# Kernel tuning notes

Measured on AMD Instinct MI355X. Metric: run time of the kernel, lower is better.

## Reference

```python
import jax, jax.numpy as jnp
import numpy as np
from jax import lax

B, C_IN, H, W = 8, 64, 256, 256
C_OUT = 128
M = 800000      # number of pixel mappings
V = 200000      # number of views (atomic groups)
N = 50000       # number of 3D points (view groups)


def _csr_ptr(key, n_seg, total):
    inner = jnp.sort(jax.random.randint(key, (n_seg - 1,), 0, total + 1, dtype=jnp.int32))
    return jnp.concatenate([jnp.zeros((1,), jnp.int32), inner,
                            jnp.full((1,), total, jnp.int32)])


def setup_inputs() -> dict:
    key = jax.random.key(0)
    k = jax.random.split(key, 7)
    x = jax.random.normal(k[0], (B, C_IN, H, W), jnp.float32)
    w = jax.random.normal(k[1], (C_OUT, C_IN, 3, 3), jnp.float32) * (1.0 / np.sqrt(C_IN * 9))
    b = jax.random.normal(k[2], (C_OUT,), jnp.float32) * 0.01
    x_3d = jax.random.normal(k[3], (N, C_OUT), jnp.float32)
    n_flat = B * (H // 2) * (W // 2)  # flattened down-conv output pixels
    fm_idx = jax.random.randint(k[4], (M,), 0, n_flat, dtype=jnp.int32)
    a_ptr = _csr_ptr(k[5], V, M)
    v_ptr = _csr_ptr(k[6], N, V)
    return {"x": x, "w": w, "b": b, "x_3d": x_3d,
            "fm_idx": fm_idx, "a_ptr": a_ptr, "v_ptr": v_ptr}


def _csr_segment_max(feats, ptr, num_segments):
    # CSR pointers -> per-row segment ids (jit-safe), then segment max.
    seg = jnp.searchsorted(ptr, jnp.arange(feats.shape[0], dtype=ptr.dtype), side='right') - 1
    out = jax.ops.segment_max(feats, seg, num_segments=num_segments)
    return jnp.where(jnp.isfinite(out), out, 0.0)  # empty segments -> 0


def reference(x, w, b, x_3d, fm_idx, a_ptr, v_ptr):
    # conv down (stride 2, pad 1) + ReLU
    y = lax.conv_general_dilated(x, w, (2, 2), ((1, 1), (1, 1)),
                                 dimension_numbers=('NCHW', 'OIHW', 'NCHW'))
    y = jax.nn.relu(y + b[None, :, None, None])
    # feature map indexing: flat gather of mapped pixels -> [M, C]
    flat = y.transpose(0, 2, 3, 1).reshape(-1, y.shape[1])
    g = flat[fm_idx]
    # atomic pool: pixels -> views (CSR segment max)
    xv = _csr_segment_max(g, a_ptr, V)
    # view pool: views -> 3D points (CSR segment max)
    xp = _csr_segment_max(xv, v_ptr, N)
    # additive fusion
    return x_3d + xp
```

## Files before the change

### kernel.cpp

```cpp
#include <hip/hip_runtime.h>
#include <hip/hip_bf16.h>


#define B_IMG  8
#define C_IN   64
#define H_IN   256
#define W_IN   256
#define C_OUT  128
#define OH     128
#define OW     128
#define NPIX   (B_IMG * OH * OW)
#define KTOT   576
#define N_PTS  50000

#define HP     258
#define PLANE  (129 * 64)
#define HROW   (2 * PLANE)

typedef __bf16 bf16x8 __attribute__((ext_vector_type(8)));
typedef float  f32x4  __attribute__((ext_vector_type(4)));

typedef unsigned int __attribute__((address_space(3))) u32_lds;
typedef unsigned int __attribute__((address_space(1))) u32_glb;

#define GLOAD_LDS16(gsrc, ldst)                                                \
  __builtin_amdgcn_global_load_lds((const u32_glb*)(gsrc),                     \
                                   (u32_lds*)(ldst), 16, 0, 0)

#define XTP_BYTES   (B_IMG * HP * HROW * 2)
#define G_BYTES     (NPIX * C_OUT * 2)
#define XTP_OFF     0
#define G_OFF       XTP_BYTES
#define WT2_OFF     (XTP_BYTES + G_BYTES)

__global__ __launch_bounds__(256) void zero_ws_kernel(uint4* __restrict__ p, long n16) {
  long i = (long)blockIdx.x * blockDim.x + threadIdx.x;
  long stride = (long)gridDim.x * blockDim.x;
  uint4 z = make_uint4(0u, 0u, 0u, 0u);
  for (; i < n16; i += stride) p[i] = z;
}

__global__ __launch_bounds__(256) void transpose_x_kernel(
    const float* __restrict__ x, __hip_bfloat16* __restrict__ xtp) {
  __shared__ __hip_bfloat16 tile[64][66];
  const int tid = threadIdx.x;
  const int w0  = blockIdx.x * 64;
  const int h   = blockIdx.y;
  const int b   = blockIdx.z;

  const int wl  = tid & 63;
  const int ci4 = tid >> 6;
  for (int cc = 0; cc < 16; ++cc) {
    int ci = cc * 4 + ci4;
    float v = x[(((long)(b * C_IN + ci) * H_IN) + h) * W_IN + w0 + wl];
    tile[ci][wl] = (__hip_bfloat16)v;
  }
  __syncthreads();
  const int cl  = tid & 63;
  const int wo4 = tid >> 6;
  const long rowbase = ((long)(b * HP) + h + 1) * HROW;
  for (int wc = 0; wc < 16; ++wc) {
    int wloc = wc * 4 + wo4;
    int pc   = w0 + wloc + 1;
    xtp[rowbase + (pc & 1) * PLANE + (pc >> 1) * 64 + cl] = tile[cl][wloc];
  }
}

__global__ __launch_bounds__(256) void wprep_kernel(
    const float* __restrict__ w, __hip_bfloat16* __restrict__ wt2b) {
  int tid  = blockIdx.x * 256 + threadIdx.x;
  int khkw = tid >> 13;
  int cout = (tid >> 6) & 127;
  int ci   = tid & 63;
  wt2b[tid] = (__hip_bfloat16)w[(cout * C_IN + ci) * 9 + khkw];
}

__global__ __launch_bounds__(256) void conv_gemm_kernel(
    const __hip_bfloat16* __restrict__ xtp,
    const __hip_bfloat16* __restrict__ wt2b,
    const float* __restrict__ bias,
    __hip_bfloat16* __restrict__ g) {
  __shared__ __hip_bfloat16 Abuf[2][8192];
  __shared__ __hip_bfloat16 Bbuf[2][8192];

  const int tid  = threadIdx.x;
  const int lane = tid & 63;
  const int wid  = tid >> 6;
  const int bid  = blockIdx.x;
  const int bimg = bid >> 7;
  const int oh   = bid & 127;
  const int wr   = wid >> 1;
  const int wc   = wid & 1;

  f32x4 acc[4][4] = {};

  auto stage = [&](int buf, int t) {
    const int kh = t / 3;
    const int kw = t - kh * 3;
    const long abase = (((long)bimg * HP + (2 * oh + kh)) * 2 + (kw & 1)) * PLANE
                       + ((kw == 2) ? 64 : 0);
    const long bbase = (long)t * 8192;
    for (int p = 0; p < 4; ++p) {
      int flat = p * 256 + tid;
      int row  = flat >> 3;
      int cs   = (flat & 7) ^ (row & 7);
      long soff = (long)row * 64 + cs * 8;
      char* dA = (char*)&Abuf[buf][0] + flat * 16;
      char* dB = (char*)&Bbuf[buf][0] + flat * 16;
      GLOAD_LDS16(xtp + abase + soff, dA);
      GLOAD_LDS16(wt2b + bbase + soff, dB);
    }
  };

  auto compute = [&](int buf) {
    const int r15 = lane & 15;
    const int kg  = lane >> 4;
    for (int h = 0; h < 2; ++h) {
      bf16x8 af[4], bfv[4];
      const int co = h * 4 + kg;
      for (int i = 0; i < 4; ++i) {
        int rowa = wr * 64 + i * 16 + r15;
        int ca   = co ^ (rowa & 7);
        af[i] = *(const bf16x8*)((const char*)&Abuf[buf][0] + rowa * 128 + ca * 16);
        int rowb = wc * 64 + i * 16 + r15;
        int cb   = co ^ (rowb & 7);
        bfv[i] = *(const bf16x8*)((const char*)&Bbuf[buf][0] + rowb * 128 + cb * 16);
      }
      for (int i = 0; i < 4; ++i)
        for (int n = 0; n < 4; ++n)
          acc[i][n] = __builtin_amdgcn_mfma_f32_16x16x32_bf16(af[i], bfv[n],
                                                              acc[i][n], 0, 0, 0);
    }
  };

  stage(0, 0);
  __syncthreads();
  int cur = 0;
  for (int t = 0; t < 9; ++t) {
    if (t + 1 < 9) stage(cur ^ 1, t + 1);
    compute(cur);
    __syncthreads();
    cur ^= 1;
  }

  __hip_bfloat16* ct = &Abuf[0][0];
  const int col0 = wc * 64 + (lane & 15);
  float bn[4];
  for (int n = 0; n < 4; ++n) bn[n] = bias[col0 + n * 16];
  for (int i = 0; i < 4; ++i) {
    int row0 = wr * 64 + i * 16 + (lane >> 4) * 4;
    for (int n = 0; n < 4; ++n) {
      int cout = col0 + n * 16;
      for (int r = 0; r < 4; ++r) {
        float v = fmaxf(acc[i][n][r] + bn[n], 0.0f);
        ct[(row0 + r) * 128 + cout] = (__hip_bfloat16)v;
      }
    }
  }
  __syncthreads();
  const long gbase = (long)bid * (128 * 128);
  for (int it = 0; it < 8; ++it) {
    int flat = it * 256 + tid;
    bf16x8 v = *(const bf16x8*)((const char*)ct + flat * 16);
    *(bf16x8*)(g + gbase + (long)flat * 8) = v;
  }
}

__global__ __launch_bounds__(256) void gather_max_add_kernel(
    const __hip_bfloat16* __restrict__ g,
    const float* __restrict__ x3d,
    const int* __restrict__ fm_idx,
    const int* __restrict__ a_ptr,
    const int* __restrict__ v_ptr,
    float* __restrict__ out) {
  const int lane = threadIdx.x & 63;
  const int n    = blockIdx.x * 4 + (threadIdx.x >> 6);

  const int v0 = v_ptr[n];
  const int v1 = v_ptr[n + 1];
  const int r0 = a_ptr[v0];
  const int r1 = a_ptr[v1];
  const int len = r1 - r0;

  const int sub  = lane >> 4;
  const int ch16 = lane & 15;

  float m[8];
#pragma unroll
  for (int k = 0; k < 8; ++k) m[k] = 0.0f;

  const uint4* gp = (const uint4*)g;

  for (int base = 0; base < len; base += 64) {
    int nb = len - base;
    if (nb > 64) nb = 64;
    int li = base + lane;
    if (li >= len) li = len - 1;
    const int idx_l = fm_idx[r0 + li];

    for (int j = 0; j < nb; j += 8) {
      int ra = j + sub;
      int rb = j + 4 + sub;
      if (ra >= nb) ra = nb - 1;
      if (rb >= nb) rb = nb - 1;
      int ia = __shfl(idx_l, ra);
      int ib = __shfl(idx_l, rb);
      uint4 va = gp[(long)ia * 16 + ch16];
      uint4 vb = gp[(long)ib * 16 + ch16];
      const unsigned* ua = (const unsigned*)&va;
      const unsigned* ub = (const unsigned*)&vb;
#pragma unroll
      for (int w = 0; w < 4; ++w) {
        m[2 * w]     = fmaxf(m[2 * w],     __uint_as_float(ua[w] << 16));
        m[2 * w + 1] = fmaxf(m[2 * w + 1], __uint_as_float(ua[w] & 0xffff0000u));
        m[2 * w]     = fmaxf(m[2 * w],     __uint_as_float(ub[w] << 16));
        m[2 * w + 1] = fmaxf(m[2 * w + 1], __uint_as_float(ub[w] & 0xffff0000u));
      }
    }
  }

#pragma unroll
  for (int k = 0; k < 8; ++k) {
    m[k] = fmaxf(m[k], __shfl_xor(m[k], 16));
    m[k] = fmaxf(m[k], __shfl_xor(m[k], 32));
  }

  if (sub == 0) {
    const float4* x4 = (const float4*)x3d;
    float4* o4 = (float4*)out;
    long b0 = (long)n * 32 + ch16 * 2;
    float4 xa = x4[b0];
    float4 xb = x4[b0 + 1];
    float4 oa, ob;
    oa.x = xa.x + m[0]; oa.y = xa.y + m[1]; oa.z = xa.z + m[2]; oa.w = xa.w + m[3];
    ob.x = xb.x + m[4]; ob.y = xb.y + m[5]; ob.z = xb.z + m[6]; ob.w = xb.w + m[7];
    o4[b0]     = oa;
    o4[b0 + 1] = ob;
  }
}

extern "C" void kernel_launch(void* const* d_in, const int* in_sizes, int n_in,
                              void* d_out, int out_size, void* d_ws, size_t ws_size,
                              hipStream_t stream) {
  const float* x     = (const float*)d_in[0];
  const float* w     = (const float*)d_in[1];
  const float* bias  = (const float*)d_in[2];
  const float* x3d   = (const float*)d_in[3];
  const int*   fmidx = (const int*)d_in[4];
  const int*   aptr  = (const int*)d_in[5];
  const int*   vptr  = (const int*)d_in[6];
  float* out = (float*)d_out;

  char* ws = (char*)d_ws;
  __hip_bfloat16* xtp  = (__hip_bfloat16*)(ws + XTP_OFF);
  __hip_bfloat16* g    = (__hip_bfloat16*)(ws + G_OFF);
  __hip_bfloat16* wt2b = (__hip_bfloat16*)(ws + WT2_OFF);

  long n16 = XTP_BYTES / 16;
  hipLaunchKernelGGL(zero_ws_kernel, dim3(4096), dim3(256), 0, stream,
                     (uint4*)xtp, n16);
  hipLaunchKernelGGL(transpose_x_kernel, dim3(W_IN / 64, H_IN, B_IMG), dim3(256),
                     0, stream, x, xtp);
  hipLaunchKernelGGL(wprep_kernel, dim3((C_OUT * KTOT) / 256), dim3(256), 0,
                     stream, w, wt2b);
  hipLaunchKernelGGL(conv_gemm_kernel, dim3(NPIX / 128), dim3(256), 0, stream,
                     xtp, wt2b, bias, g);
  hipLaunchKernelGGL(gather_max_add_kernel, dim3(N_PTS / 4), dim3(256), 0,
                     stream, g, x3d, fmidx, aptr, vptr, out);
}
```

Measured before the change: 304.4 us.

## Zero only halo, pack transpose stores, widen conv blocks, split gather across warps

Replaces the full workspace zeroing with a kernel that clears only the padding rows and columns. The input transpose now packs two bf16 channels into 32-bit LDS and global stores. The conv GEMM uses 512-thread blocks with 8 waves, each owning a 64x32 output tile instead of 64x64. The gather/segment-max kernel assigns one block per 3D point, splits the rows across four waves, and reduces the partial maxima through shared memory. Together these aim to cut redundant memory traffic and raise parallelism, at the cost of more blocks and an extra sync in the gather.

After: 346.0 us. +13.7%, slower.

```diff
diff --git a/kernel.cpp b/kernel.cpp
--- a/kernel.cpp
+++ b/kernel.cpp
@@ -33,36 +33,49 @@
 #define G_OFF       XTP_BYTES
 #define WT2_OFF     (XTP_BYTES + G_BYTES)
 
-__global__ __launch_bounds__(256) void zero_ws_kernel(uint4* __restrict__ p, long n16) {
-  long i = (long)blockIdx.x * blockDim.x + threadIdx.x;
-  long stride = (long)gridDim.x * blockDim.x;
+__global__ __launch_bounds__(256) void halo_zero_kernel(__hip_bfloat16* __restrict__ xtp) {
+  const int ph = blockIdx.x;
+  const int b  = blockIdx.y;
+  const int tid = threadIdx.x;
+  const long base = ((long)b * HP + ph) * HROW;
   uint4 z = make_uint4(0u, 0u, 0u, 0u);
-  for (; i < n16; i += stride) p[i] = z;
+  uint4* p = (uint4*)(xtp + base);
+  if (ph == 0 || ph == HP - 1) {
+    for (int i = tid; i < (HROW * 2) / 16; i += 256) p[i] = z;
+  } else {
+    if (tid < 8) p[tid] = z;
+    else if (tid < 16) ((uint4*)(xtp + base + PLANE + 128 * 64))[tid - 8] = z;
+  }
 }
 
 __global__ __launch_bounds__(256) void transpose_x_kernel(
-    const float* __restrict__ x, __hip_bfloat16* __restrict__ xtp) {
-  __shared__ __hip_bfloat16 tile[64][66];
+    const float* __restrict__ x, unsigned* __restrict__ xtp32) {
+  __shared__ unsigned tile32[32][65];
   const int tid = threadIdx.x;
   const int w0  = blockIdx.x * 64;
   const int h   = blockIdx.y;
   const int b   = blockIdx.z;
 
-  const int wl  = tid & 63;
-  const int ci4 = tid >> 6;
-  for (int cc = 0; cc < 16; ++cc) {
-    int ci = cc * 4 + ci4;
-    float v = x[(((long)(b * C_IN + ci) * H_IN) + h) * W_IN + w0 + wl];
-    tile[ci][wl] = (__hip_bfloat16)v;
-  }
-  __syncthreads();
-  const int cl  = tid & 63;
-  const int wo4 = tid >> 6;
-  const long rowbase = ((long)(b * HP) + h + 1) * HROW;
-  for (int wc = 0; wc < 16; ++wc) {
-    int wloc = wc * 4 + wo4;
+  const int wl = tid & 63;
+  const int c4 = tid >> 6;
+  for (int cc = 0; cc < 8; ++cc) {
+    int cpair = cc * 4 + c4;
+    const float* xr = x + (((long)(b * C_IN + 2 * cpair) * H_IN) + h) * W_IN + w0;
+    float v0 = xr[wl];
+    float v1 = xr[(long)H_IN * W_IN + wl];
+    unsigned u0 = __builtin_bit_cast(unsigned short, (__bf16)v0);
+    unsigned u1 = __builtin_bit_cast(unsigned short, (__bf16)v1);
+    tile32[cpair][wl] = u0 | (u1 << 16);
+  }
+  __syncthreads();
+  const int cpair = tid & 31;
+  const int ws0   = tid >> 5;
+  const long rowb2 = (((long)(b * HP) + h + 1) * HROW) >> 1;
+  for (int it = 0; it < 8; ++it) {
+    int wloc = it * 8 + ws0;
     int pc   = w0 + wloc + 1;
-    xtp[rowbase + (pc & 1) * PLANE + (pc >> 1) * 64 + cl] = tile[cl][wloc];
+    xtp32[rowb2 + (pc & 1) * (PLANE >> 1) + (pc >> 1) * 32 + cpair] =
+        tile32[cpair][wloc];
   }
 }
 
@@ -75,7 +88,7 @@
   wt2b[tid] = (__hip_bfloat16)w[(cout * C_IN + ci) * 9 + khkw];
 }
 
-__global__ __launch_bounds__(256) void conv_gemm_kernel(
+__global__ __launch_bounds__(512) void conv_gemm_kernel(
     const __hip_bfloat16* __restrict__ xtp,
     const __hip_bfloat16* __restrict__ wt2b,
     const float* __restrict__ bias,
@@ -89,10 +102,10 @@
   const int bid  = blockIdx.x;
   const int bimg = bid >> 7;
   const int oh   = bid & 127;
-  const int wr   = wid >> 1;
-  const int wc   = wid & 1;
-
-  f32x4 acc[4][4] = {};
+  const int wr   = wid >> 2;
+  const int wc   = wid & 3;
+
+  f32x4 acc[4][2] = {};
 
   auto stage = [&](int buf, int t) {
     const int kh = t / 3;
@@ -100,8 +113,8 @@
     const long abase = (((long)bimg * HP + (2 * oh + kh)) * 2 + (kw & 1)) * PLANE
                        + ((kw == 2) ? 64 : 0);
     const long bbase = (long)t * 8192;
-    for (int p = 0; p < 4; ++p) {
-      int flat = p * 256 + tid;
+    for (int p = 0; p < 2; ++p) {
+      int flat = p * 512 + tid;
       int row  = flat >> 3;
       int cs   = (flat & 7) ^ (row & 7);
       long soff = (long)row * 64 + cs * 8;
@@ -116,18 +129,20 @@
     const int r15 = lane & 15;
     const int kg  = lane >> 4;
     for (int h = 0; h < 2; ++h) {
-      bf16x8 af[4], bfv[4];
+      bf16x8 af[4], bfv[2];
       const int co = h * 4 + kg;
       for (int i = 0; i < 4; ++i) {
         int rowa = wr * 64 + i * 16 + r15;
         int ca   = co ^ (rowa & 7);
         af[i] = *(const bf16x8*)((const char*)&Abuf[buf][0] + rowa * 128 + ca * 16);
-        int rowb = wc * 64 + i * 16 + r15;
+      }
+      for (int n = 0; n < 2; ++n) {
+        int rowb = wc * 32 + n * 16 + r15;
         int cb   = co ^ (rowb & 7);
-        bfv[i] = *(const bf16x8*)((const char*)&Bbuf[buf][0] + rowb * 128 + cb * 16);
+        bfv[n] = *(const bf16x8*)((const char*)&Bbuf[buf][0] + rowb * 128 + cb * 16);
       }
       for (int i = 0; i < 4; ++i)
-        for (int n = 0; n < 4; ++n)
+        for (int n = 0; n < 2; ++n)
           acc[i][n] = __builtin_amdgcn_mfma_f32_16x16x32_bf16(af[i], bfv[n],
                                                               acc[i][n], 0, 0, 0);
     }
@@ -144,12 +159,12 @@
   }
 
   __hip_bfloat16* ct = &Abuf[0][0];
-  const int col0 = wc * 64 + (lane & 15);
-  float bn[4];
-  for (int n = 0; n < 4; ++n) bn[n] = bias[col0 + n * 16];
+  const int col0 = wc * 32 + (lane & 15);
+  float bn[2];
+  for (int n = 0; n < 2; ++n) bn[n] = bias[col0 + n * 16];
   for (int i = 0; i < 4; ++i) {
     int row0 = wr * 64 + i * 16 + (lane >> 4) * 4;
-    for (int n = 0; n < 4; ++n) {
+    for (int n = 0; n < 2; ++n) {
       int cout = col0 + n * 16;
       for (int r = 0; r < 4; ++r) {
         float v = fmaxf(acc[i][n][r] + bn[n], 0.0f);
@@ -159,8 +174,8 @@
   }
   __syncthreads();
   const long gbase = (long)bid * (128 * 128);
-  for (int it = 0; it < 8; ++it) {
-    int flat = it * 256 + tid;
+  for (int it = 0; it < 4; ++it) {
+    int flat = it * 512 + tid;
     bf16x8 v = *(const bf16x8*)((const char*)ct + flat * 16);
     *(bf16x8*)(g + gbase + (long)flat * 8) = v;
   }
@@ -173,8 +188,11 @@
     const int* __restrict__ a_ptr,
     const int* __restrict__ v_ptr,
     float* __restrict__ out) {
-  const int lane = threadIdx.x & 63;
-  const int n    = blockIdx.x * 4 + (threadIdx.x >> 6);
+  __shared__ float red[4][128];
+  const int tid  = threadIdx.x;
+  const int lane = tid & 63;
+  const int wid  = tid >> 6;
+  const int n    = blockIdx.x;
 
   const int v0 = v_ptr[n];
   const int v1 = v_ptr[n + 1];
@@ -191,7 +209,7 @@
 
   const uint4* gp = (const uint4*)g;
 
-  for (int base = 0; base < len; base += 64) {
+  for (int base = wid * 64; base < len; base += 256) {
     int nb = len - base;
     if (nb > 64) nb = 64;
     int li = base + lane;
@@ -224,18 +242,16 @@
     m[k] = fmaxf(m[k], __shfl_xor(m[k], 16));
     m[k] = fmaxf(m[k], __shfl_xor(m[k], 32));
   }
-
   if (sub == 0) {
-    const float4* x4 = (const float4*)x3d;
-    float4* o4 = (float4*)out;
-    long b0 = (long)n * 32 + ch16 * 2;
-    float4 xa = x4[b0];
-    float4 xb = x4[b0 + 1];
-    float4 oa, ob;
-    oa.x = xa.x + m[0]; oa.y = xa.y + m[1]; oa.z = xa.z + m[2]; oa.w = xa.w + m[3];
-    ob.x = xb.x + m[4]; ob.y = xb.y + m[5]; ob.z = xb.z + m[6]; ob.w = xb.w + m[7];
-    o4[b0]     = oa;
-    o4[b0 + 1] = ob;
+#pragma unroll
+    for (int k = 0; k < 8; ++k) red[wid][ch16 * 8 + k] = m[k];
+  }
+  __syncthreads();
+
+  if (tid < 128) {
+    float v = fmaxf(fmaxf(red[0][tid], red[1][tid]),
+                    fmaxf(red[2][tid], red[3][tid]));
+    out[(long)n * 128 + tid] = x3d[(long)n * 128 + tid] + v;
   }
 }
 
@@ -256,15 +272,14 @@
   __hip_bfloat16* g    = (__hip_bfloat16*)(ws + G_OFF);
   __hip_bfloat16* wt2b = (__hip_bfloat16*)(ws + WT2_OFF);
 
-  long n16 = XTP_BYTES / 16;
-  hipLaunchKernelGGL(zero_ws_kernel, dim3(4096), dim3(256), 0, stream,
-                     (uint4*)xtp, n16);
+  hipLaunchKernelGGL(halo_zero_kernel, dim3(HP, B_IMG), dim3(256), 0, stream,
+                     xtp);
   hipLaunchKernelGGL(transpose_x_kernel, dim3(W_IN / 64, H_IN, B_IMG), dim3(256),
-                     0, stream, x, xtp);
+                     0, stream, x, (unsigned*)xtp);
   hipLaunchKernelGGL(wprep_kernel, dim3((C_OUT * KTOT) / 256), dim3(256), 0,
                      stream, w, wt2b);
-  hipLaunchKernelGGL(conv_gemm_kernel, dim3(NPIX / 128), dim3(256), 0, stream,
+  hipLaunchKernelGGL(conv_gemm_kernel, dim3(NPIX / 128), dim3(512), 0, stream,
                      xtp, wt2b, bias, g);
-  hipLaunchKernelGGL(gather_max_add_kernel, dim3(N_PTS / 4), dim3(256), 0,
+  hipLaunchKernelGGL(gather_max_add_kernel, dim3(N_PTS), dim3(256), 0,
                      stream, g, x3d, fmidx, aptr, vptr, out);
 }
```
